# Kernel tuning notes

Hardware: AMD Instinct MI355X
Metric: run time of the kernel (lower is better)

Reference implementation:

```python
import jax, jax.numpy as jnp
from jax import lax
import numpy as np

INPUT_DIM = 1024; ENT_DIM = 256; KEY_DIM = 32; FUNC_DIM = 256; HID = 32
NUM_LAYERS = 1; UNIT_TYPE_DIM = 259; MAX_ENT = 64; B = 256; N = 512
NEG = 1e9

def _ln(x, g, b, eps=1e-5):
    m = x.mean(-1, keepdims=True)
    v = ((x - m) ** 2).mean(-1, keepdims=True)
    return (x - m) / jnp.sqrt(v + eps) * g + b

def setup_inputs() -> dict:
    key = jax.random.key(0)
    ks = jax.random.split(key, 16)
    def lin(k, i, o, s=0.02):
        return jax.random.normal(k, (i, o), jnp.float32) * s, jnp.zeros((o,), jnp.float32)
    p = {}
    p['key_fc_w'], p['key_fc_b'] = lin(ks[0], ENT_DIM, KEY_DIM)
    p['func_fc_w'], p['func_fc_b'] = lin(ks[1], UNIT_TYPE_DIM, FUNC_DIM)
    p['fc1_w'], p['fc1_b'] = lin(ks[2], INPUT_DIM, FUNC_DIM)
    p['fc2_w'], p['fc2_b'] = lin(ks[3], FUNC_DIM, KEY_DIM)
    p['embed_fc_w'], p['embed_fc_b'] = lin(ks[4], KEY_DIM, INPUT_DIM)
    p['lstm_wx'] = jax.random.normal(ks[5], (NUM_LAYERS, KEY_DIM, 4 * HID), jnp.float32) * 0.05
    p['lstm_wh'] = jax.random.normal(ks[6], (NUM_LAYERS, HID, 4 * HID), jnp.float32) * 0.05
    p['lstm_b'] = jnp.zeros((NUM_LAYERS, 4 * HID), jnp.float32)
    p['lstm_ln_gx'] = jnp.ones((NUM_LAYERS, 4 * HID), jnp.float32)
    p['lstm_ln_bx'] = jnp.zeros((NUM_LAYERS, 4 * HID), jnp.float32)
    p['lstm_ln_gh'] = jnp.ones((NUM_LAYERS, 4 * HID), jnp.float32)
    p['lstm_ln_bh'] = jnp.zeros((NUM_LAYERS, 4 * HID), jnp.float32)
    inp = {
        'embedding': jax.random.normal(ks[7], (B, INPUT_DIM), jnp.float32),
        'available_unit_type_mask': (jax.random.uniform(ks[8], (B, UNIT_TYPE_DIM)) < 0.5).astype(jnp.float32),
        'available_units_mask': jnp.ones((B, N), jnp.float32),
        'entity_embedding': jax.random.normal(ks[9], (B, N, ENT_DIM), jnp.float32),
        'temperature': jnp.float32(1.0),
    }
    inp.update(p)
    return inp

def reference(embedding, available_unit_type_mask, available_units_mask, entity_embedding,
              temperature, key_fc_w, key_fc_b, func_fc_w, func_fc_b, fc1_w, fc1_b,
              fc2_w, fc2_b, embed_fc_w, embed_fc_b, lstm_wx, lstm_wh, lstm_b,
              lstm_ln_gx, lstm_ln_bx, lstm_ln_gh, lstm_ln_bh):
    relu = jax.nn.relu
    # _get_key: [B,N,KEY] + end-flag row of zeros -> [B,N+1,KEY]
    key = entity_embedding @ key_fc_w + key_fc_b
    key = jnp.concatenate([key, jnp.zeros((B, 1, KEY_DIM), key.dtype)], axis=1)
    end_idx = N
    # _get_init_query
    func_embed = relu(available_unit_type_mask @ func_fc_w + func_fc_b)
    x0 = relu(embedding @ fc1_w + fc1_b)
    x0 = relu((x0 + func_embed) @ fc2_w + fc2_b)  # [B, KEY_DIM]
    mask0 = jnp.concatenate([available_units_mask, jnp.ones((B, 1), available_units_mask.dtype)], axis=1)

    h0 = jnp.zeros((NUM_LAYERS, B, HID), key.dtype)
    c0 = jnp.zeros((NUM_LAYERS, B, HID), key.dtype)
    units0 = jnp.zeros((B, N + 1), jnp.int32)
    done0 = jnp.zeros((B,), bool)
    rng0 = jax.random.key(42)

    def step(carry, _):
        x, h, c, mask, units, done, rng = carry
        xi = x
        hs, cs = [], []
        for l in range(NUM_LAYERS):  # LN-LSTM, gate order i,f,o,u (DI-engine)
            gate = (_ln(xi @ lstm_wx[l], lstm_ln_gx[l], lstm_ln_bx[l])
                    + _ln(h[l] @ lstm_wh[l], lstm_ln_gh[l], lstm_ln_bh[l]) + lstm_b[l])
            i_g, f_g, o_g, u_g = jnp.split(gate, 4, axis=-1)
            cl = jax.nn.sigmoid(f_g) * c[l] + jax.nn.sigmoid(i_g) * jnp.tanh(u_g)
            hl = jax.nn.sigmoid(o_g) * jnp.tanh(cl)
            hs.append(hl); cs.append(cl); xi = hl
        h_new = jnp.stack(hs); c_new = jnp.stack(cs)
        q = (xi[:, None, :] * key).mean(-1)          # [B, N+1] pointer scores
        q = q - (1.0 - mask) * NEG
        rng, sk = jax.random.split(rng)
        idx = jax.random.categorical(sk, q / temperature, axis=-1)  # [B]
        is_end = idx == end_idx
        active = jnp.logical_not(done)
        sel = active & jnp.logical_not(is_end)
        onehot = jax.nn.one_hot(idx, N + 1, dtype=mask.dtype)
        units = jnp.where(sel[:, None] & (onehot > 0.5), 1, units)
        mask = jnp.where(sel[:, None], mask * (1.0 - onehot), mask)
        done = done | (active & is_end)
        return (xi, h_new, c_new, mask, units, done, rng), (q, active)

    carry, (logits, valid) = lax.scan(step, (x0, h0, c0, mask0, units0, done0, rng0), None, length=MAX_ENT)
    units = carry[4]
    emb_sel = (units[..., None].astype(key.dtype) * key).mean(axis=1)  # [B, KEY_DIM]
    emb_sel = emb_sel @ embed_fc_w + embed_fc_b
    return logits, valid, units, embedding + emb_sel
```

## Files before the change

### kernel.cpp

```cpp
#include <hip/hip_runtime.h>
#include <stdint.h>
#include <stddef.h>

#define JAX_PARTITIONABLE 1

#define B_   256
#define N_   512
#define NP_  513
#define KROW 516
#define T_   64
#define CS   4
#define NCH  16
#define NEGC 1e9f

__host__ __device__ __forceinline__ void tf2x32(uint32_t k0, uint32_t k1,
    uint32_t x0, uint32_t x1, uint32_t& o0, uint32_t& o1) {
  const uint32_t k2 = k0 ^ k1 ^ 0x1BD11BDAu;
#define TFR(r) { x0 += x1; x1 = (x1 << (r)) | (x1 >> (32 - (r))); x1 ^= x0; }
  x0 += k0; x1 += k1;
  TFR(13) TFR(15) TFR(26) TFR(6)
  x0 += k1; x1 += k2 + 1u;
  TFR(17) TFR(29) TFR(16) TFR(24)
  x0 += k2; x1 += k0 + 2u;
  TFR(13) TFR(15) TFR(26) TFR(6)
  x0 += k0; x1 += k1 + 3u;
  TFR(17) TFR(29) TFR(16) TFR(24)
  x0 += k1; x1 += k2 + 4u;
  TFR(13) TFR(15) TFR(26) TFR(6)
  x0 += k2; x1 += k0 + 5u;
#undef TFR
  o0 = x0; o1 = x1;
}

struct SkKeys { uint32_t k[128]; };

static SkKeys compute_chain() {
  SkKeys s;
  uint32_t r0 = 0u, r1 = 42u;
  for (int t = 0; t < 64; ++t) {
#if JAX_PARTITIONABLE
    uint32_t a0, a1, b0, b1;
    tf2x32(r0, r1, 0u, 0u, a0, a1);
    tf2x32(r0, r1, 0u, 1u, b0, b1);
    s.k[2*t] = b0; s.k[2*t+1] = b1;
    r0 = a0; r1 = a1;
#else
    uint32_t p0, p1, q0, q1;
    tf2x32(r0, r1, 0u, 2u, p0, p1);
    tf2x32(r0, r1, 1u, 3u, q0, q1);
    s.k[2*t] = p1; s.k[2*t+1] = q1;
    r0 = p0; r1 = q0;
#endif
  }
  return s;
}

__device__ __forceinline__ float gumbel_draw(uint32_t k0, uint32_t k1, int b, int n) {
  uint32_t bits;
#if JAX_PARTITIONABLE
  uint32_t j = (uint32_t)(b * NP_ + n);
  uint32_t o0, o1; tf2x32(k0, k1, 0u, j, o0, o1);
  bits = o0 ^ o1;
#else
  int j = b * NP_ + n;
  uint32_t o0, o1;
  if (j < 65664) { tf2x32(k0, k1, (uint32_t)j, (uint32_t)(j + 65664), o0, o1); bits = o0; }
  else           { tf2x32(k0, k1, (uint32_t)(j - 65664), (uint32_t)j, o0, o1); bits = o1; }
#endif
  float f = __uint_as_float((bits >> 9) | 0x3F800000u) - 1.0f;
  const float TINY = 1.17549435e-38f;
  float u = fmaxf(TINY, f + TINY);
  return -logf(-logf(u));
}

__device__ __forceinline__ float sigm(float x) {
  return 0.5f + 0.5f * tanhf(0.5f * x);
}

__device__ __forceinline__ void bar_lds() {
  asm volatile("s_waitcnt lgkmcnt(0)\n\ts_barrier" ::: "memory");
}

#define WS_KEY 0
#define WS_X0  (B_ * 32 * KROW)
#define WS_H   (WS_X0 + B_ * 32)

__global__ void __launch_bounds__(512, 2)
k_pre(const float* __restrict__ emb, const float* __restrict__ autm,
      const float* __restrict__ ent,
      const float* __restrict__ key_w, const float* __restrict__ key_b,
      const float* __restrict__ func_w, const float* __restrict__ func_b,
      const float* __restrict__ fc1_w, const float* __restrict__ fc1_b,
      const float* __restrict__ fc2_w, const float* __restrict__ fc2_b,
      float* __restrict__ ws)
{
  __shared__ float smT[256];
  const int b   = blockIdx.x;
  const int tid = threadIdx.x;

  if (tid < 256) {
    float a = 0.f;
    const float* e = emb + (size_t)b * 1024;
    #pragma unroll 8
    for (int k = 0; k < 1024; ++k) a += e[k] * fc1_w[k * 256 + tid];
    a = fmaxf(a + fc1_b[tid], 0.f);
    float f = 0.f;
    const float* m = autm + (size_t)b * 259;
    for (int k = 0; k < 259; ++k) f += m[k] * func_w[k * 256 + tid];
    f = fmaxf(f + func_b[tid], 0.f);
    smT[tid] = a + f;
  } else {
    const int i = tid - 256;
    const float4* kw4 = (const float4*)key_w;
    #pragma unroll 1
    for (int rnd = 0; rnd < 2; ++rnd) {
      const int n = i + rnd * 256;
      const float4* er = (const float4*)(ent + ((size_t)b * N_ + n) * 256);
      float acc[32];
      #pragma unroll
      for (int c = 0; c < 32; ++c) acc[c] = 0.f;
      #pragma unroll 4
      for (int k4 = 0; k4 < 64; ++k4) {
        float4 ev = er[k4];
        float e4[4] = {ev.x, ev.y, ev.z, ev.w};
        #pragma unroll
        for (int j = 0; j < 4; ++j) {
          const int k = k4 * 4 + j;
          #pragma unroll
          for (int c4 = 0; c4 < 8; ++c4) {
            float4 w = kw4[k * 8 + c4];
            acc[c4*4+0] += e4[j] * w.x;
            acc[c4*4+1] += e4[j] * w.y;
            acc[c4*4+2] += e4[j] * w.z;
            acc[c4*4+3] += e4[j] * w.w;
          }
        }
      }
      #pragma unroll
      for (int c = 0; c < 32; ++c)
        ws[WS_KEY + ((size_t)(b * 32 + c)) * KROW + n] = acc[c] + key_b[c];
    }
    if (i < 32) ws[WS_KEY + ((size_t)(b * 32 + i)) * KROW + N_] = 0.f;
  }
  __syncthreads();

  if (tid < 32) {
    float s = 0.f;
    #pragma unroll 8
    for (int m2 = 0; m2 < 256; ++m2) s += smT[m2] * fc2_w[m2 * 32 + tid];
    ws[WS_X0 + b * 32 + tid] = fmaxf(s + fc2_b[tid], 0.f);
  }
}

__global__ void __launch_bounds__(64, 1)
k_beta(const float* __restrict__ wx, const float* __restrict__ wh,
       const float* __restrict__ lstm_bb,
       const float* __restrict__ ln_gx, const float* __restrict__ ln_bx,
       const float* __restrict__ ln_gh, const float* __restrict__ ln_bh,
       float* __restrict__ ws)
{
  const int b   = blockIdx.x;
  const int tid = threadIdx.x;

  float wxr0[32], wxr1[32], whr0[32], whr1[32];
  #pragma unroll
  for (int k = 0; k < 32; ++k) {
    wxr0[k] = wx[k * 128 + tid];
    wxr1[k] = wx[k * 128 + 64 + tid];
    whr0[k] = wh[k * 128 + tid];
    whr1[k] = wh[k * 128 + 64 + tid];
  }
  #pragma unroll
  for (int k = 0; k < 32; ++k) {
    asm volatile("" : "+v"(wxr0[k]), "+v"(wxr1[k]), "+v"(whr0[k]), "+v"(whr1[k]));
  }
  const float gxg0 = ln_gx[tid], gxg1 = ln_gx[tid + 64];
  const float gxb0 = ln_bx[tid], gxb1 = ln_bx[tid + 64];
  const float ghg0 = ln_gh[tid], ghg1 = ln_gh[tid + 64];
  const float ghb0 = ln_bh[tid], ghb1 = ln_bh[tid + 64];
  const float lb0  = lstm_bb[tid], lb1 = lstm_bb[tid + 64];

  float xf[32];
  {
    const float* x0g = ws + WS_X0 + b * 32;
    #pragma unroll
    for (int r = 0; r < 8; ++r) {
      float4 v = *(const float4*)(x0g + r * 4);
      xf[r*4] = v.x; xf[r*4+1] = v.y; xf[r*4+2] = v.z; xf[r*4+3] = v.w;
    }
  }
  float creg = 0.f;
  float* Hout = ws + WS_H + (size_t)b * (T_ * 32);

  #pragma unroll 1
  for (int t = 0; t < T_; ++t) {
    float a0 = 0.f, a1 = 0.f, b0 = 0.f, b1 = 0.f;
    #pragma unroll
    for (int k = 0; k < 32; ++k) { a0 += xf[k] * wxr0[k]; a1 += xf[k] * wxr1[k]; }
    if (t > 0) {
      #pragma unroll
      for (int k = 0; k < 32; ++k) { b0 += xf[k] * whr0[k]; b1 += xf[k] * whr1[k]; }
    }
    float sx = a0 + a1, sh = b0 + b1;
    for (int off = 32; off; off >>= 1) {
      sx += __shfl_down(sx, off);
      sh += __shfl_down(sh, off);
    }
    float mx  = __shfl(sx, 0) * (1.0f / 128.0f);
    float mh2 = __shfl(sh, 0) * (1.0f / 128.0f);
    float dx0 = a0 - mx, dx1 = a1 - mx;
    float dh0 = b0 - mh2, dh1 = b1 - mh2;
    float ssx = dx0 * dx0 + dx1 * dx1;
    float ssh = dh0 * dh0 + dh1 * dh1;
    for (int off = 32; off; off >>= 1) {
      ssx += __shfl_down(ssx, off);
      ssh += __shfl_down(ssh, off);
    }
    float vx = __shfl(ssx, 0) * (1.0f / 128.0f);
    float vh = __shfl(ssh, 0) * (1.0f / 128.0f);
    float rx = 1.0f / sqrtf(vx + 1e-5f);
    float rh = 1.0f / sqrtf(vh + 1e-5f);
    float lnx0 = dx0 * rx * gxg0 + gxb0;
    float lnx1 = dx1 * rx * gxg1 + gxb1;
    float lnh0 = dh0 * rh * ghg0 + ghb0;
    float lnh1 = dh1 * rh * ghg1 + ghb1;
    float g0 = lnx0 + lnh0 + lb0;
    float g1 = lnx1 + lnh1 + lb1;
    float fq = __shfl(g0, tid + 32);
    float uq = __shfl(g1, tid + 32);
    float cN = sigm(fq) * creg + sigm(g0) * tanhf(uq);
    float hN = sigm(g1) * tanhf(cN);
    creg = cN;
    if (tid < 32) Hout[t * 32 + tid] = hN;
    #pragma unroll
    for (int k = 0; k < 32; ++k) xf[k] = __shfl(hN, k);
  }
}

#define OFF_KEY   0
#define OFF_H     16512
#define OFF_Q     18560
#define OFF_G     22688
#define OFF_UNITS 33008
#define OFF_SK    33524
#define OFF_ES    33652
#define OFF_PART  33684
#define LDS_FLOATS 34196

__global__ void __launch_bounds__(512, 2)
k_sample(const float* __restrict__ ws_ro,
         const float* __restrict__ aum, const float* __restrict__ temp_p,
         const float* __restrict__ emb,
         const float* __restrict__ emb_w, const float* __restrict__ emb_b,
         float* __restrict__ out_logits, float* __restrict__ out_valid,
         float* __restrict__ out_units, float* __restrict__ out_final,
         SkKeys sk)
{
  extern __shared__ __align__(16) float sm[];
  int* smi = (int*)sm;
  const int b   = blockIdx.x;
  const int tid = threadIdx.x;
  const int L   = tid - 64;

  const float temp = temp_p[0];

  {
    const float4* kv = (const float4*)(ws_ro + WS_KEY + (size_t)b * (32 * KROW));
    for (int i = tid; i < (32 * KROW) / 4; i += 512) ((float4*)sm)[i] = kv[i];
    const float4* hv = (const float4*)(ws_ro + WS_H + (size_t)b * (T_ * 32));
    if (tid < 512) ((float4*)(sm + OFF_H))[tid] = hv[tid];
    if (tid < 128) smi[OFF_SK + tid] = (int)sk.k[tid];
  }
  __syncthreads();

  float kr0[32], kr1[32];
  float mreg[8], ureg[8];
  float m512 = 1.0f;
  int done_reg = 0;

  auto qprep = [&](int cc, int qs) {
    const int qb = OFF_Q + qs * (CS * 516);
    #pragma unroll 1
    for (int tl = 0; tl < CS; ++tl) {
      const int hb = OFF_H + (cc * CS + tl) * 32;
      float hv[32];
      #pragma unroll
      for (int r = 0; r < 8; ++r) {
        float4 v = *(const float4*)&sm[hb + r * 4];
        hv[r*4] = v.x; hv[r*4+1] = v.y; hv[r*4+2] = v.z; hv[r*4+3] = v.w;
      }
      float a0 = 0.f;
      #pragma unroll
      for (int k = 0; k < 32; ++k) a0 += hv[k] * kr0[k];
      sm[qb + tl * 516 + L] = a0 * (1.0f / 32.0f);
      if (L < 64) {
        float a1 = 0.f;
        #pragma unroll
        for (int k = 0; k < 32; ++k) a1 += hv[k] * kr1[k];
        sm[qb + tl * 516 + L + 448] = a1 * (1.0f / 32.0f);
      }
    }
  };
  auto gprep = [&](int cc, int gs) {
    const int gb = OFF_G + gs * (CS * 516);
    #pragma unroll 1
    for (int i = 0; i < 5; ++i) {
      const int idx = i * 448 + L;
      if (idx < CS * 512) {
        const int tl = idx >> 9, n = idx & 511;
        const int t = cc * CS + tl;
        sm[gb + tl * 516 + n] =
            gumbel_draw((uint32_t)smi[OFF_SK + 2*t], (uint32_t)smi[OFF_SK + 2*t + 1], b, n);
      }
    }
    if (L < CS) {
      const int t = cc * CS + L;
      sm[gb + L * 516 + N_] =
          gumbel_draw((uint32_t)smi[OFF_SK + 2*t], (uint32_t)smi[OFF_SK + 2*t + 1], b, N_);
    }
  };

  if (tid < 64) {
    #pragma unroll
    for (int j = 0; j < 8; ++j) {
      mreg[j] = aum[(size_t)b * N_ + tid + 64 * j];
      ureg[j] = 0.f;
    }
  } else {
    #pragma unroll
    for (int c = 0; c < 32; ++c) kr0[c] = sm[OFF_KEY + c * KROW + L];
    if (L < 64) {
      #pragma unroll
      for (int c = 0; c < 32; ++c) kr1[c] = sm[OFF_KEY + c * KROW + L + 448];
    }
    #pragma unroll 1
    for (int cc = 0; cc < 4; ++cc) gprep(cc, cc);
    qprep(0, 0);
  }
  bar_lds();

  for (int c = 0; c < NCH; ++c) {
    if (tid < 64) {
      const int qbase = OFF_Q + (c & 1) * (CS * 516);
      const int gbase = OFF_G + (c % 5) * (CS * 516);
      #pragma unroll 1
      for (int tl = 0; tl < CS; ++tl) {
        const int t = c * CS + tl;
        float* lrow = out_logits + ((size_t)t * B_ + b) * NP_;
        float bv = 0.f; int bi = 0;
        #pragma unroll
        for (int j = 0; j < 8; ++j) {
          const int n = tid + 64 * j;
          float q = sm[qbase + tl * 516 + n] - (1.0f - mreg[j]) * NEGC;
          lrow[n] = q;
          float v = q / temp + sm[gbase + tl * 516 + n];
          if (j == 0) { bv = v; bi = n; }
          else if (v > bv) { bv = v; bi = n; }
        }
        if (tid == 0) {
          float q = -(1.0f - m512) * NEGC;
          lrow[N_] = q;
          float v = q / temp + sm[gbase + tl * 516 + N_];
          if (v > bv) { bv = v; bi = N_; }
        }
        for (int off = 32; off; off >>= 1) {
          float ov = __shfl_down(bv, off);
          int   oi = __shfl_down(bi, off);
          if (ov > bv || (ov == bv && oi < bi)) { bv = ov; bi = oi; }
        }
        const int sel_i = __shfl(bi, 0);
        const int active = !done_reg;
        const int is_end = (sel_i == N_);
        if (tid == 0) out_valid[(size_t)t * B_ + b] = active ? 1.0f : 0.0f;
        if (active && !is_end) {
          #pragma unroll
          for (int j = 0; j < 8; ++j)
            if (tid + 64 * j == sel_i) { mreg[j] = 0.0f; ureg[j] = 1.0f; }
        }
        if (active && is_end) done_reg = 1;
      }
    } else {
      if (c + 1 < NCH) qprep(c + 1, (c + 1) & 1);
      if (c + 4 < NCH) gprep(c + 4, (c + 4) % 5);
    }
    bar_lds();
  }

  if (tid < 64) {
    #pragma unroll
    for (int j = 0; j < 8; ++j) sm[OFF_UNITS + tid + 64 * j] = ureg[j];
    if (tid == 0) sm[OFF_UNITS + N_] = 0.f;
  }
  __syncthreads();

  {
    const int g = tid >> 5, cc = tid & 31;
    float p = 0.f;
    const int n0 = g * 32;
    for (int nn = 0; nn < 32; ++nn) {
      const int n = n0 + nn;
      p += sm[OFF_UNITS + n] * sm[OFF_KEY + cc * KROW + n];
    }
    if (g == 15) p += sm[OFF_UNITS + N_] * sm[OFF_KEY + cc * KROW + N_];
    sm[OFF_PART + g * 32 + cc] = p;
  }
  for (int n = tid; n < NP_; n += 512) out_units[(size_t)b * NP_ + n] = sm[OFF_UNITS + n];
  __syncthreads();
  if (tid < 32) {
    float s = 0.f;
    #pragma unroll
    for (int g = 0; g < 16; ++g) s += sm[OFF_PART + g * 32 + tid];
    sm[OFF_ES + tid] = s / 513.0f;
  }
  __syncthreads();
  {
    const float* e = emb + (size_t)b * 1024;
    for (int d = tid; d < 1024; d += 512) {
      float a = 0.f;
      #pragma unroll
      for (int k = 0; k < 32; ++k) a += sm[OFF_ES + k] * emb_w[k * 1024 + d];
      out_final[(size_t)b * 1024 + d] = e[d] + a + emb_b[d];
    }
  }
}

extern "C" void kernel_launch(void* const* d_in, const int* in_sizes, int n_in,
                              void* d_out, int out_size, void* d_ws, size_t ws_size,
                              hipStream_t stream) {
  (void)in_sizes; (void)n_in; (void)ws_size; (void)out_size;
  const float* emb    = (const float*)d_in[0];
  const float* autm   = (const float*)d_in[1];
  const float* aum    = (const float*)d_in[2];
  const float* ent    = (const float*)d_in[3];
  const float* temp   = (const float*)d_in[4];
  const float* key_w  = (const float*)d_in[5];
  const float* key_b  = (const float*)d_in[6];
  const float* func_w = (const float*)d_in[7];
  const float* func_b = (const float*)d_in[8];
  const float* fc1_w  = (const float*)d_in[9];
  const float* fc1_b  = (const float*)d_in[10];
  const float* fc2_w  = (const float*)d_in[11];
  const float* fc2_b  = (const float*)d_in[12];
  const float* emb_w  = (const float*)d_in[13];
  const float* emb_b  = (const float*)d_in[14];
  const float* wx     = (const float*)d_in[15];
  const float* wh     = (const float*)d_in[16];
  const float* lb     = (const float*)d_in[17];
  const float* gxg    = (const float*)d_in[18];
  const float* gxb    = (const float*)d_in[19];
  const float* ghg    = (const float*)d_in[20];
  const float* ghb    = (const float*)d_in[21];
  float* out = (float*)d_out;
  float* ws  = (float*)d_ws;

  const size_t OFF_V = (size_t)T_ * B_ * NP_;
  const size_t OFF_U = OFF_V + (size_t)T_ * B_;
  const size_t OFF_F = OFF_U + (size_t)B_ * NP_;

  SkKeys sk = compute_chain();

  k_pre<<<dim3(B_), dim3(512), 0, stream>>>(
      emb, autm, ent, key_w, key_b, func_w, func_b,
      fc1_w, fc1_b, fc2_w, fc2_b, ws);

  k_beta<<<dim3(B_), dim3(64), 0, stream>>>(
      wx, wh, lb, gxg, gxb, ghg, ghb, ws);

  k_sample<<<dim3(B_), dim3(512), LDS_FLOATS * sizeof(float), stream>>>(
      ws, aum, temp, emb, emb_w, emb_b,
      out, out + OFF_V, out + OFF_U, out + OFF_F, sk);
}
```

Before: 299.5 us.

## Fuse pre-projection and LSTM kernels, tile key projection across extra blocks

Merges the preprocessing kernel and the LSTM recurrence kernel into one launch with 1280 blocks. The first 256 blocks compute the fc1/func/fc2 path and then run the LSTM directly from LDS. The remaining 1024 blocks compute the entity key projection as an LDS-tiled 128x32 GEMM with 4x4 register tiles. The LSTM hidden-state broadcast now goes through LDS instead of 32 shuffles. The aim is to spread the key GEMM over more blocks, cut one kernel launch, and drop the x0 round trip through global memory, at the cost of divergent block roles and larger LDS use.

```diff
diff --git a/kernel.cpp b/kernel.cpp
--- a/kernel.cpp
+++ b/kernel.cpp
@@ -80,25 +80,97 @@
 __device__ __forceinline__ void bar_lds() {
   asm volatile("s_waitcnt lgkmcnt(0)\n\ts_barrier" ::: "memory");
 }
+__device__ __forceinline__ void lds_fence() {
+  asm volatile("s_waitcnt lgkmcnt(0)" ::: "memory");
+}
 
 #define WS_KEY 0
 #define WS_X0  (B_ * 32 * KROW)
 #define WS_H   (WS_X0 + B_ * 32)
 
-__global__ void __launch_bounds__(512, 2)
-k_pre(const float* __restrict__ emb, const float* __restrict__ autm,
-      const float* __restrict__ ent,
-      const float* __restrict__ key_w, const float* __restrict__ key_b,
-      const float* __restrict__ func_w, const float* __restrict__ func_b,
-      const float* __restrict__ fc1_w, const float* __restrict__ fc1_b,
-      const float* __restrict__ fc2_w, const float* __restrict__ fc2_b,
-      float* __restrict__ ws)
+__global__ void __launch_bounds__(256)
+k_front(const float* __restrict__ emb, const float* __restrict__ autm,
+        const float* __restrict__ ent,
+        const float* __restrict__ key_w, const float* __restrict__ key_b,
+        const float* __restrict__ func_w, const float* __restrict__ func_b,
+        const float* __restrict__ fc1_w, const float* __restrict__ fc1_b,
+        const float* __restrict__ fc2_w, const float* __restrict__ fc2_b,
+        const float* __restrict__ wx, const float* __restrict__ wh,
+        const float* __restrict__ lstm_bb,
+        const float* __restrict__ ln_gx, const float* __restrict__ ln_bx,
+        const float* __restrict__ ln_gh, const float* __restrict__ ln_bh,
+        float* __restrict__ ws)
 {
-  __shared__ float smT[256];
-  const int b   = blockIdx.x;
+  __shared__ __align__(16) float smAll[16384];
   const int tid = threadIdx.x;
 
-  if (tid < 256) {
+  if (blockIdx.x >= 256) {
+    float* smA = smAll;
+    float* smW = smAll + 8192;
+    const int blk = blockIdx.x - 256;
+    const int R0  = blk * 128;
+    const int b   = R0 >> 9;
+    const int nb  = R0 & 511;
+    const int rg  = tid >> 3;
+    const int cg  = tid & 7;
+
+    for (int i = tid; i < 2048; i += 256)
+      ((float4*)smW)[i] = ((const float4*)key_w)[i];
+
+    float acc[4][4];
+    #pragma unroll
+    for (int i = 0; i < 4; ++i)
+      #pragma unroll
+      for (int j = 0; j < 4; ++j) acc[i][j] = 0.f;
+
+    const int row  = tid >> 1;
+    const int half = tid & 1;
+
+    for (int kc = 0; kc < 4; ++kc) {
+      const float4* src = (const float4*)(ent + ((size_t)(R0 + row)) * 256 + kc * 64 + half * 32);
+      float4 vv[8];
+      #pragma unroll
+      for (int r = 0; r < 8; ++r) vv[r] = src[r];
+      #pragma unroll
+      for (int r = 0; r < 8; ++r) {
+        const int kl = half * 32 + r * 4;
+        smA[(kl + 0) * 128 + row] = vv[r].x;
+        smA[(kl + 1) * 128 + row] = vv[r].y;
+        smA[(kl + 2) * 128 + row] = vv[r].z;
+        smA[(kl + 3) * 128 + row] = vv[r].w;
+      }
+      __syncthreads();
+      #pragma unroll 4
+      for (int k = 0; k < 64; ++k) {
+        float4 av = *(const float4*)&smA[k * 128 + rg * 4];
+        float4 bv = *(const float4*)&smW[(kc * 64 + k) * 32 + cg * 4];
+        float ar[4] = {av.x, av.y, av.z, av.w};
+        float br[4] = {bv.x, bv.y, bv.z, bv.w};
+        #pragma unroll
+        for (int i = 0; i < 4; ++i)
+          #pragma unroll
+          for (int j = 0; j < 4; ++j) acc[i][j] += ar[i] * br[j];
+      }
+      __syncthreads();
+    }
+    float4 bb = *(const float4*)&key_b[cg * 4];
+    float bbr[4] = {bb.x, bb.y, bb.z, bb.w};
+    #pragma unroll
+    for (int j = 0; j < 4; ++j) {
+      const int c = cg * 4 + j;
+      float* dst = ws + WS_KEY + ((size_t)(b * 32 + c)) * KROW + nb + rg * 4;
+      #pragma unroll
+      for (int i = 0; i < 4; ++i) dst[i] = acc[i][j] + bbr[j];
+    }
+    return;
+  }
+
+  const int b = blockIdx.x;
+  float* smT  = smAll;
+  float* smX0 = smAll + 256;
+  float* smHB = smAll + 288;
+
+  {
     float a = 0.f;
     const float* e = emb + (size_t)b * 1024;
     #pragma unroll 8
@@ -109,58 +181,18 @@
     for (int k = 0; k < 259; ++k) f += m[k] * func_w[k * 256 + tid];
     f = fmaxf(f + func_b[tid], 0.f);
     smT[tid] = a + f;
-  } else {
-    const int i = tid - 256;
-    const float4* kw4 = (const float4*)key_w;
-    #pragma unroll 1
-    for (int rnd = 0; rnd < 2; ++rnd) {
-      const int n = i + rnd * 256;
-      const float4* er = (const float4*)(ent + ((size_t)b * N_ + n) * 256);
-      float acc[32];
-      #pragma unroll
-      for (int c = 0; c < 32; ++c) acc[c] = 0.f;
-      #pragma unroll 4
-      for (int k4 = 0; k4 < 64; ++k4) {
-        float4 ev = er[k4];
-        float e4[4] = {ev.x, ev.y, ev.z, ev.w};
-        #pragma unroll
-        for (int j = 0; j < 4; ++j) {
-          const int k = k4 * 4 + j;
-          #pragma unroll
-          for (int c4 = 0; c4 < 8; ++c4) {
-            float4 w = kw4[k * 8 + c4];
-            acc[c4*4+0] += e4[j] * w.x;
-            acc[c4*4+1] += e4[j] * w.y;
-            acc[c4*4+2] += e4[j] * w.z;
-            acc[c4*4+3] += e4[j] * w.w;
-          }
-        }
-      }
-      #pragma unroll
-      for (int c = 0; c < 32; ++c)
-        ws[WS_KEY + ((size_t)(b * 32 + c)) * KROW + n] = acc[c] + key_b[c];
-    }
-    if (i < 32) ws[WS_KEY + ((size_t)(b * 32 + i)) * KROW + N_] = 0.f;
   }
   __syncthreads();
-
   if (tid < 32) {
     float s = 0.f;
     #pragma unroll 8
     for (int m2 = 0; m2 < 256; ++m2) s += smT[m2] * fc2_w[m2 * 32 + tid];
-    ws[WS_X0 + b * 32 + tid] = fmaxf(s + fc2_b[tid], 0.f);
-  }
-}
-
-__global__ void __launch_bounds__(64, 1)
-k_beta(const float* __restrict__ wx, const float* __restrict__ wh,
-       const float* __restrict__ lstm_bb,
-       const float* __restrict__ ln_gx, const float* __restrict__ ln_bx,
-       const float* __restrict__ ln_gh, const float* __restrict__ ln_bh,
-       float* __restrict__ ws)
-{
-  const int b   = blockIdx.x;
-  const int tid = threadIdx.x;
+    smX0[tid] = fmaxf(s + fc2_b[tid], 0.f);
+  }
+  if (tid >= 64 && tid < 96)
+    ws[WS_KEY + ((size_t)(b * 32 + (tid - 64))) * KROW + N_] = 0.f;
+  __syncthreads();
+  if (tid >= 64) return;
 
   float wxr0[32], wxr1[32], whr0[32], whr1[32];
   #pragma unroll
@@ -181,13 +213,10 @@
   const float lb0  = lstm_bb[tid], lb1 = lstm_bb[tid + 64];
 
   float xf[32];
-  {
-    const float* x0g = ws + WS_X0 + b * 32;
-    #pragma unroll
-    for (int r = 0; r < 8; ++r) {
-      float4 v = *(const float4*)(x0g + r * 4);
-      xf[r*4] = v.x; xf[r*4+1] = v.y; xf[r*4+2] = v.z; xf[r*4+3] = v.w;
-    }
+  #pragma unroll
+  for (int r = 0; r < 8; ++r) {
+    float4 v = *(const float4*)&smX0[r * 4];
+    xf[r*4] = v.x; xf[r*4+1] = v.y; xf[r*4+2] = v.z; xf[r*4+3] = v.w;
   }
   float creg = 0.f;
   float* Hout = ws + WS_H + (size_t)b * (T_ * 32);
@@ -231,9 +260,13 @@
     float cN = sigm(fq) * creg + sigm(g0) * tanhf(uq);
     float hN = sigm(g1) * tanhf(cN);
     creg = cN;
-    if (tid < 32) Hout[t * 32 + tid] = hN;
-    #pragma unroll
-    for (int k = 0; k < 32; ++k) xf[k] = __shfl(hN, k);
+    if (tid < 32) { Hout[t * 32 + tid] = hN; smHB[tid] = hN; }
+    lds_fence();
+    #pragma unroll
+    for (int r = 0; r < 8; ++r) {
+      float4 v = *(const float4*)&smHB[r * 4];
+      xf[r*4] = v.x; xf[r*4+1] = v.y; xf[r*4+2] = v.z; xf[r*4+3] = v.w;
+    }
   }
 }
 
@@ -459,11 +492,9 @@
 
   SkKeys sk = compute_chain();
 
-  k_pre<<<dim3(B_), dim3(512), 0, stream>>>(
+  k_front<<<dim3(1280), dim3(256), 0, stream>>>(
       emb, autm, ent, key_w, key_b, func_w, func_b,
-      fc1_w, fc1_b, fc2_w, fc2_b, ws);
-
-  k_beta<<<dim3(B_), dim3(64), 0, stream>>>(
+      fc1_w, fc1_b, fc2_w, fc2_b,
       wx, wh, lb, gxg, gxb, ghg, ghb, ws);
 
   k_sample<<<dim3(B_), dim3(512), LDS_FLOATS * sizeof(float), stream>>>(
```

After: 255.7 us. -14.6%, faster.
